# Performance work log

Measured on AMD Instinct MI355X. Metric: run time of the kernel, lower is better.

## Reference

```python
import jax, jax.numpy as jnp
import numpy as np

EPS = 1e-6

def setup_inputs() -> dict:
    key = jax.random.key(0)
    k1, k2 = jax.random.split(key)
    pred_map = jax.random.uniform(k1, (64, 512, 512), dtype=jnp.float32)
    true_map = jax.random.uniform(k2, (64, 512, 512), dtype=jnp.float32)
    return {"pred_map": pred_map, "true_map": true_map}

def reference(pred_map, true_map):
    # per-sample normalize over all non-batch dims, then KL(true || pred), mean over batch
    B = pred_map.shape[0]
    pred = (pred_map + EPS).reshape(B, -1)
    true = (true_map + EPS).reshape(B, -1)
    pred = pred / jnp.sum(pred, axis=1, keepdims=True)
    true = true / jnp.sum(true, axis=1, keepdims=True)
    kl = jnp.sum(true * jnp.log(true / pred), axis=1)  # [B]
    return jnp.mean(kl)
```

## Files before the change

kernel.cpp:

```cpp
#include <hip/hip_runtime.h>
#include <hip/hip_bf16.h>

#define EPS 1e-6f

typedef float f4 __attribute__((ext_vector_type(4)));

constexpr int B = 64;
constexpr int NPB = 512 * 512;
constexpr int BLOCKS_PER_BATCH = 32;
constexpr int NBLK = B * BLOCKS_PER_BATCH;
constexpr int THREADS = 256;
constexpr int CHUNK = NPB / BLOCKS_PER_BATCH;
constexpr int ITERS = CHUNK / 4 / THREADS;

__device__ __forceinline__ float waveReduce(float v) {
    #pragma unroll
    for (int off = 32; off > 0; off >>= 1) v += __shfl_down(v, off, 64);
    return v;
}

__global__ __launch_bounds__(THREADS) void kl_partial(
        const float* __restrict__ pred, const float* __restrict__ truem,
        float* __restrict__ ws) {
    const size_t base = (size_t)blockIdx.x * CHUNK;
    const f4* p4 = (const f4*)(pred + base);
    const f4* t4 = (const f4*)(truem + base);

    float sp = 0.f, st = 0.f, s = 0.f;
    #pragma unroll
    for (int j = 0; j < ITERS; ++j) {
        f4 p = __builtin_nontemporal_load(&p4[threadIdx.x + j * THREADS]);
        f4 t = __builtin_nontemporal_load(&t4[threadIdx.x + j * THREADS]);
        sp += (p.x + p.y) + (p.z + p.w);
        st += (t.x + t.y) + (t.z + t.w);
        float px = p.x + EPS, py = p.y + EPS, pz = p.z + EPS, pw = p.w + EPS;
        float tx = t.x + EPS, ty = t.y + EPS, tz = t.z + EPS, tw = t.w + EPS;
        s += tx * (__logf(tx) - __logf(px));
        s += ty * (__logf(ty) - __logf(py));
        s += tz * (__logf(tz) - __logf(pz));
        s += tw * (__logf(tw) - __logf(pw));
    }

    sp = waveReduce(sp);
    st = waveReduce(st);
    s  = waveReduce(s);

    __shared__ float red[3][THREADS / 64];
    const int wave = threadIdx.x >> 6;
    const int lane = threadIdx.x & 63;
    if (lane == 0) { red[0][wave] = sp; red[1][wave] = st; red[2][wave] = s; }
    __syncthreads();
    if (threadIdx.x == 0) {
        float a0 = 0.f, a1 = 0.f, a2 = 0.f;
        #pragma unroll
        for (int w = 0; w < THREADS / 64; ++w) {
            a0 += red[0][w]; a1 += red[1][w]; a2 += red[2][w];
        }
        ws[blockIdx.x]            = a0;
        ws[NBLK + blockIdx.x]     = a1;
        ws[2 * NBLK + blockIdx.x] = a2;
    }
}

__global__ __launch_bounds__(64) void kl_final(
        const float* __restrict__ ws, float* __restrict__ out) {
    const int b = threadIdx.x;
    float Sp = 0.f, St = 0.f, S = 0.f;
    #pragma unroll
    for (int k = 0; k < BLOCKS_PER_BATCH; ++k) {
        const int idx = b * BLOCKS_PER_BATCH + k;
        Sp += ws[idx];
        St += ws[NBLK + idx];
        S  += ws[2 * NBLK + idx];
    }
    const float epsN = (float)NPB * EPS;
    Sp += epsN;
    St += epsN;
    float kl = S / St + logf(Sp / St);
    kl = waveReduce(kl);
    if (b == 0) out[0] = kl * (1.0f / B);
}

extern "C" void kernel_launch(void* const* d_in, const int* in_sizes, int n_in,
                              void* d_out, int out_size, void* d_ws, size_t ws_size,
                              hipStream_t stream) {
    const float* pred  = (const float*)d_in[0];
    const float* truem = (const float*)d_in[1];
    float* out = (float*)d_out;
    float* ws  = (float*)d_ws;

    kl_partial<<<NBLK, THREADS, 0, stream>>>(pred, truem, ws);
    kl_final<<<1, 64, 0, stream>>>(ws, out);
}
```

Before: 137.7 us.

## Stage pred chunk into LDS via direct global-to-LDS loads, use log2

Loads each block's pred chunk asynchronously into LDS with global_load_lds while true values are loaded into registers and their t*log2(t) term is computed, then reads pred from LDS to compute the cross term. Logs switch to log2 with a single LN2 rescale in the final kernel. The aim is to overlap the two input streams and cut the log cost. In exchange it adds 32KB of LDS per block, which may lower occupancy, plus a block-wide barrier and larger register arrays for the true values.

```diff
diff --git a/kernel.cpp b/kernel.cpp
--- a/kernel.cpp
+++ b/kernel.cpp
@@ -2,6 +2,7 @@
 #include <hip/hip_bf16.h>
 
 #define EPS 1e-6f
+#define LN2 0.6931471805599453f
 
 typedef float f4 __attribute__((ext_vector_type(4)));
 
@@ -10,8 +11,8 @@
 constexpr int BLOCKS_PER_BATCH = 32;
 constexpr int NBLK = B * BLOCKS_PER_BATCH;
 constexpr int THREADS = 256;
-constexpr int CHUNK = NPB / BLOCKS_PER_BATCH;
-constexpr int ITERS = CHUNK / 4 / THREADS;
+constexpr int CHUNK = 8192;
+constexpr int F4_PER_THREAD = CHUNK / 4 / THREADS;
 
 __device__ __forceinline__ float waveReduce(float v) {
     #pragma unroll
@@ -19,35 +20,63 @@
     return v;
 }
 
+__device__ __forceinline__ void stage16(const float* g, float* l) {
+    __builtin_amdgcn_global_load_lds(
+        (const __attribute__((address_space(1))) void*)g,
+        (__attribute__((address_space(3))) void*)l, 16, 0, 0);
+}
+
 __global__ __launch_bounds__(THREADS) void kl_partial(
         const float* __restrict__ pred, const float* __restrict__ truem,
         float* __restrict__ ws) {
+    __shared__ float lds_p[CHUNK];
+
     const size_t base = (size_t)blockIdx.x * CHUNK;
-    const f4* p4 = (const f4*)(pred + base);
-    const f4* t4 = (const f4*)(truem + base);
+    const int wave = threadIdx.x >> 6;
+    const int lane = threadIdx.x & 63;
 
-    float sp = 0.f, st = 0.f, s = 0.f;
     #pragma unroll
-    for (int j = 0; j < ITERS; ++j) {
-        f4 p = __builtin_nontemporal_load(&p4[threadIdx.x + j * THREADS]);
-        f4 t = __builtin_nontemporal_load(&t4[threadIdx.x + j * THREADS]);
-        sp += (p.x + p.y) + (p.z + p.w);
-        st += (t.x + t.y) + (t.z + t.w);
-        float px = p.x + EPS, py = p.y + EPS, pz = p.z + EPS, pw = p.w + EPS;
-        float tx = t.x + EPS, ty = t.y + EPS, tz = t.z + EPS, tw = t.w + EPS;
-        s += tx * (__logf(tx) - __logf(px));
-        s += ty * (__logf(ty) - __logf(py));
-        s += tz * (__logf(tz) - __logf(pz));
-        s += tw * (__logf(tw) - __logf(pw));
+    for (int j = 0; j < 8; ++j) {
+        const int off = wave * 2048 + j * 256;
+        stage16(pred + base + off + lane * 4, lds_p + off);
     }
 
+    const f4* t4 = (const f4*)(truem + base);
+    f4 t[F4_PER_THREAD];
+    float st = 0.f, s_tt = 0.f;
+    #pragma unroll
+    for (int j = 0; j < F4_PER_THREAD; ++j) {
+        t[j] = __builtin_nontemporal_load(&t4[threadIdx.x + j * THREADS]);
+        st += (t[j].x + t[j].y) + (t[j].z + t[j].w);
+        float tx = t[j].x + EPS, ty = t[j].y + EPS;
+        float tz = t[j].z + EPS, tw = t[j].w + EPS;
+        s_tt += tx * __log2f(tx);
+        s_tt += ty * __log2f(ty);
+        s_tt += tz * __log2f(tz);
+        s_tt += tw * __log2f(tw);
+    }
+
+    __syncthreads();
+
+    const f4* lp = (const f4*)lds_p;
+    float sp = 0.f, s_tp = 0.f;
+    #pragma unroll
+    for (int j = 0; j < F4_PER_THREAD; ++j) {
+        f4 p = lp[threadIdx.x + j * THREADS];
+        sp += (p.x + p.y) + (p.z + p.w);
+        float px = p.x + EPS, py = p.y + EPS, pz = p.z + EPS, pw = p.w + EPS;
+        s_tp += (t[j].x + EPS) * __log2f(px);
+        s_tp += (t[j].y + EPS) * __log2f(py);
+        s_tp += (t[j].z + EPS) * __log2f(pz);
+        s_tp += (t[j].w + EPS) * __log2f(pw);
+    }
+
+    float s = s_tt - s_tp;
     sp = waveReduce(sp);
     st = waveReduce(st);
     s  = waveReduce(s);
 
     __shared__ float red[3][THREADS / 64];
-    const int wave = threadIdx.x >> 6;
-    const int lane = threadIdx.x & 63;
     if (lane == 0) { red[0][wave] = sp; red[1][wave] = st; red[2][wave] = s; }
     __syncthreads();
     if (threadIdx.x == 0) {
@@ -76,7 +105,7 @@
     const float epsN = (float)NPB * EPS;
     Sp += epsN;
     St += epsN;
-    float kl = S / St + logf(Sp / St);
+    float kl = (S * LN2) / St + logf(Sp / St);
     kl = waveReduce(kl);
     if (b == 0) out[0] = kl * (1.0f / B);
 }
```

New measurement: 143.6 us. 1.04x slower.
